# Kernel optimization log

Hardware: AMD Instinct MI355X
Metric: run time of the kernel (lower is better)

The kernel has to match this reference:

```python
import jax, jax.numpy as jnp
import numpy as np

B, T, C, H = 4, 2048, 1024, 16
D = C // H  # head dim = 64


def setup_inputs() -> dict:
    key = jax.random.key(0)
    ks = jax.random.split(key, 5)
    scale = 1.0 / np.sqrt(C)
    return {
        "x": jax.random.normal(ks[0], (B, T, C), dtype=jnp.float32),
        "qkv_w": jax.random.uniform(ks[1], (C, 3 * C), dtype=jnp.float32, minval=-scale, maxval=scale),
        "qkv_b": jax.random.uniform(ks[2], (3 * C,), dtype=jnp.float32, minval=-scale, maxval=scale),
        "out_w": jax.random.uniform(ks[3], (C, C), dtype=jnp.float32, minval=-scale, maxval=scale),
        "out_b": jax.random.uniform(ks[4], (C,), dtype=jnp.float32, minval=-scale, maxval=scale),
    }


def reference(x, qkv_w, qkv_b, out_w, out_b):
    b, t, c = x.shape
    qkv = x @ qkv_w + qkv_b  # [b, t, 3c]
    q, k, v = jnp.split(qkv, 3, axis=-1)
    # [b, h, t, d]
    q = q.reshape(b, t, H, D).transpose(0, 2, 1, 3)
    k = k.reshape(b, t, H, D).transpose(0, 2, 1, 3)
    v = v.reshape(b, t, H, D).transpose(0, 2, 1, 3)
    scores = jnp.einsum("bhqd,bhkd->bhqk", q, k) / jnp.sqrt(jnp.float32(D))
    causal = jnp.tril(jnp.ones((t, t), dtype=bool))
    scores = jnp.where(causal[None, None, :, :], scores, -jnp.inf)
    attn = jax.nn.softmax(scores, axis=-1)
    out = jnp.einsum("bhqk,bhkd->bhqd", attn, v)
    out = out.transpose(0, 2, 1, 3).reshape(b, t, c)
    return out @ out_w + out_b
```

## Files before the change

### kernel.cpp

```cpp
#include <hip/hip_runtime.h>
#include <type_traits>

typedef __bf16 bf16;
typedef __attribute__((ext_vector_type(8))) __bf16 bf16x8;
typedef __attribute__((ext_vector_type(4))) float f32x4;
typedef __attribute__((ext_vector_type(16))) float f32x16;

constexpr int Bc = 4, Tc = 2048, Cc = 1024, Hc = 16;
constexpr int Mrows = Bc * Tc;
constexpr int N3 = 3 * Cc;

#define GLOAD(gp, lp)                                                          \
  __builtin_amdgcn_global_load_lds(                                           \
      (const __attribute__((address_space(1))) void*)(gp),                     \
      (__attribute__((address_space(3))) void*)(lp), 16, 0, 0)

__device__ __forceinline__ uint32_t pk2(float a, float b) {
  uint16_t x = __builtin_bit_cast(uint16_t, (bf16)a);
  uint16_t y = __builtin_bit_cast(uint16_t, (bf16)b);
  return (uint32_t)x | ((uint32_t)y << 16);
}

__global__ __launch_bounds__(256) void cast_bf16_kernel(
    const float* __restrict__ in, bf16* __restrict__ out, int n8) {
  int i = blockIdx.x * blockDim.x + threadIdx.x;
  int stride = gridDim.x * blockDim.x;
  for (; i < n8; i += stride) {
    const float4* p = (const float4*)(in + (long)i * 8);
    float4 a = p[0], b = p[1];
    bf16x8 v;
    v[0] = (bf16)a.x; v[1] = (bf16)a.y; v[2] = (bf16)a.z; v[3] = (bf16)a.w;
    v[4] = (bf16)b.x; v[5] = (bf16)b.y; v[6] = (bf16)b.z; v[7] = (bf16)b.w;
    *(bf16x8*)(out + (long)i * 8) = v;
  }
}

__global__ __launch_bounds__(256) void transpose_cast_kernel(
    const float* __restrict__ in, bf16* __restrict__ out, int rows, int cols,
    float scale, int srows) {
  __shared__ float tile[32][33];
  int tx = threadIdx.x, ty = threadIdx.y;
  int r0 = blockIdx.y * 32, c0 = blockIdx.x * 32;
#pragma unroll
  for (int i = 0; i < 4; i++)
    tile[ty + 8 * i][tx] = in[(long)(r0 + ty + 8 * i) * cols + c0 + tx];
  __syncthreads();
#pragma unroll
  for (int i = 0; i < 4; i++) {
    int orow = c0 + ty + 8 * i;
    float v = tile[tx][ty + 8 * i];
    if (orow < srows) v *= scale;
    out[(long)orow * rows + r0 + tx] = (bf16)v;
  }
}

__global__ __launch_bounds__(256) void transpose_v_kernel(
    const bf16* __restrict__ Y, bf16* __restrict__ Vt) {
  __shared__ bf16 tile[32][33];
  int tx = threadIdx.x, ty = threadIdx.y;
  int t0 = blockIdx.x * 32;
  int d0 = blockIdx.y * 32;
  int bh = blockIdx.z;
  int b = bh >> 4, h = bh & 15;
  const bf16* src = Y + (long)(b * Tc) * N3 + 2 * Cc + h * 64;
#pragma unroll
  for (int i = 0; i < 4; i++)
    tile[ty + 8 * i][tx] = src[(long)(t0 + ty + 8 * i) * N3 + d0 + tx];
  __syncthreads();
  bf16* dst = Vt + (long)bh * 64 * Tc;
  int txp = (tx & 0x13) | ((tx & 4) << 1) | ((tx & 8) >> 1);
#pragma unroll
  for (int i = 0; i < 4; i++)
    dst[(long)(d0 + ty + 8 * i) * Tc + t0 + txp] = tile[tx][ty + 8 * i];
}

template <typename OutT>
__global__ __launch_bounds__(256) void gemm_bt_kernel(
    const bf16* __restrict__ A, const bf16* __restrict__ Bt,
    const float* __restrict__ bias, OutT* __restrict__ Cout, int M, int N,
    int K, int sb) {
  __shared__ __align__(16) bf16 Alds[128 * 32];
  __shared__ __align__(16) bf16 Blds[128 * 32];
  const int tid = threadIdx.x;
  const int w = tid >> 6, l = tid & 63;
  const int m0 = blockIdx.x * 128, n0 = blockIdx.y * 128;
  const int wr = w >> 1, wc = w & 1;
  f32x4 acc[4][4] = {};
  const int arow = tid >> 2, achunk = tid & 3;
  const bf16* Ag = A + (long)(m0 + arow) * K + achunk * 8;
  const bf16* Bg = Bt + (long)(n0 + arow) * K + achunk * 8;
  char* AldsB = (char*)Alds;
  char* BldsB = (char*)Blds;
  const int wbase = w * 1024;

  for (int k0 = 0; k0 < K; k0 += 32) {
    __syncthreads();
    GLOAD(Ag + k0, AldsB + wbase);
    GLOAD(Ag + k0 + (long)64 * K, AldsB + wbase + 4096);
    GLOAD(Bg + k0, BldsB + wbase);
    GLOAD(Bg + k0 + (long)64 * K, BldsB + wbase + 4096);
    __syncthreads();
    const int kk = (l >> 4) * 8;
    bf16x8 af[4], bfr[4];
#pragma unroll
    for (int mi = 0; mi < 4; mi++)
      af[mi] = *(const bf16x8*)(AldsB +
                                ((wr * 64 + mi * 16 + (l & 15)) * 32 + kk) * 2);
#pragma unroll
    for (int ni = 0; ni < 4; ni++)
      bfr[ni] = *(const bf16x8*)(BldsB +
                                 ((wc * 64 + ni * 16 + (l & 15)) * 32 + kk) * 2);
#pragma unroll
    for (int mi = 0; mi < 4; mi++)
#pragma unroll
      for (int ni = 0; ni < 4; ni++)
        acc[mi][ni] = __builtin_amdgcn_mfma_f32_16x16x32_bf16(
            af[mi], bfr[ni], acc[mi][ni], 0, 0, 0);
  }
  const int rrow = (l >> 4) * 4, col = l & 15;
#pragma unroll
  for (int mi = 0; mi < 4; mi++) {
#pragma unroll
    for (int ni = 0; ni < 4; ni++) {
      int gcol = n0 + wc * 64 + ni * 16 + col;
      float bv = bias[gcol];
      if (gcol < sb) bv *= 0.125f;
#pragma unroll
      for (int i = 0; i < 4; i++) {
        int grow = m0 + wr * 64 + mi * 16 + rrow + i;
        float v = acc[mi][ni][i] + bv;
        if constexpr (std::is_same<OutT, float>::value)
          Cout[(long)grow * N + gcol] = v;
        else
          Cout[(long)grow * N + gcol] = (bf16)v;
      }
    }
  }
}

__global__ __launch_bounds__(256) void flash_kernel(
    const bf16* __restrict__ Y, const bf16* __restrict__ Vt,
    bf16* __restrict__ O) {
  __shared__ __align__(16) bf16 Klds[2][64 * 64];
  __shared__ __align__(16) bf16 Vlds[2][64 * 64];
  const int tid = threadIdx.x;
  const int w = tid >> 6, l = tid & 63;
  const int ln = l & 31, hi = l >> 5;
  const int bh = blockIdx.y;
  const int b = bh >> 4, h = bh & 15;
  const bf16* Kbase = Y + (long)(b * Tc) * N3 + Cc + h * 64;
  const bf16* Vbase = Vt + (long)bh * 64 * Tc;

  const int srow = tid >> 3, schunk = tid & 7;
  const int swz = (schunk ^ (srow & 7)) * 8;
  const int wbase = w * 1024;
  char* KldsB = (char*)Klds;
  char* VldsB = (char*)Vlds;

  auto stage = [&](int buf, int kt0) {
    char* kd = KldsB + buf * 8192 + wbase;
    char* vd = VldsB + buf * 8192 + wbase;
    GLOAD(Kbase + (long)(kt0 + srow) * N3 + swz, kd);
    GLOAD(Kbase + (long)(kt0 + srow + 32) * N3 + swz, kd + 4096);
    GLOAD(Vbase + (long)srow * Tc + kt0 + swz, vd);
    GLOAD(Vbase + (long)(srow + 32) * Tc + kt0 + swz, vd + 4096);
  };

#pragma unroll 1
  for (int sp = 0; sp < 2; sp++) {
    const int st = sp ? (15 - (int)blockIdx.x) : (int)blockIdx.x;
    const int q0 = st * 128;
    const int qmin = q0 + w * 32;
    const int qg = qmin + ln;
    const long grow = (long)(b * Tc) + qg;

    bf16x8 aq[4];
#pragma unroll
    for (int dc = 0; dc < 4; dc++)
      aq[dc] = *(const bf16x8*)(Y + grow * N3 + h * 64 + dc * 16 + hi * 8);

    f32x16 ot[2] = {};
    float mrun = -__builtin_inff(), lrun = 0.f;
    const int nkt = 2 * st + 2;

    stage(0, 0);
    __syncthreads();

    for (int kt = 0; kt < nkt; kt++) {
      const int kt0 = kt * 64;
      if (kt + 1 < nkt) stage((kt + 1) & 1, kt0 + 64);
      const char* kb = KldsB + (kt & 1) * 8192;
      const char* vb = VldsB + (kt & 1) * 8192;

      if (kt0 <= qmin + 31) {
        f32x16 s[2];
#pragma unroll
        for (int ks = 0; ks < 2; ks++) {
          f32x16 acc = {};
          const int krow = ks * 32 + ln;
          const int kswz = (krow & 7) << 4;
#pragma unroll
          for (int dc = 0; dc < 4; dc++) {
            bf16x8 ak =
                *(const bf16x8*)(kb + krow * 128 + ((dc * 32 + hi * 16) ^ kswz));
            acc = __builtin_amdgcn_mfma_f32_32x32x16_bf16(ak, aq[dc], acc, 0, 0, 0);
          }
          s[ks] = acc;
        }
        if (kt0 + 63 > qmin) {
#pragma unroll
          for (int ks = 0; ks < 2; ks++)
#pragma unroll
            for (int r = 0; r < 16; r++) {
              int kg = kt0 + ks * 32 + (r & 3) + 8 * (r >> 2) + 4 * hi;
              if (kg > qg) s[ks][r] = -__builtin_inff();
            }
        }
        float tm = s[0][0];
#pragma unroll
        for (int ks = 0; ks < 2; ks++)
#pragma unroll
          for (int r = 0; r < 16; r++) tm = fmaxf(tm, s[ks][r]);
        tm = fmaxf(tm, __shfl_xor(tm, 32));
        float mnew = fmaxf(mrun, tm);
        float factor = __expf(mrun - mnew);
        float lsum = 0.f;
#pragma unroll
        for (int ks = 0; ks < 2; ks++)
#pragma unroll
          for (int r = 0; r < 16; r++) {
            float p = __expf(s[ks][r] - mnew);
            s[ks][r] = p;
            lsum += p;
          }
        lsum += __shfl_xor(lsum, 32);
        lrun = lrun * factor + lsum;
        mrun = mnew;
#pragma unroll
        for (int db = 0; db < 2; db++)
#pragma unroll
          for (int r = 0; r < 16; r++) ot[db][r] *= factor;
        uint32_t pu[2][8];
#pragma unroll
        for (int ks = 0; ks < 2; ks++)
#pragma unroll
          for (int j = 0; j < 8; j++)
            pu[ks][j] = pk2(s[ks][2 * j], s[ks][2 * j + 1]);
#pragma unroll
        for (int ks = 0; ks < 2; ks++)
#pragma unroll
          for (int g = 0; g < 2; g++) {
            union { uint32_t u[4]; bf16x8 v; } pf;
            pf.u[0] = pu[ks][g * 4 + 0];
            pf.u[1] = pu[ks][g * 4 + 1];
            pf.u[2] = pu[ks][g * 4 + 2];
            pf.u[3] = pu[ks][g * 4 + 3];
#pragma unroll
            for (int db = 0; db < 2; db++) {
              const int vrow = db * 32 + ln;
              bf16x8 av = *(const bf16x8*)(
                  vb + vrow * 128 +
                  ((ks * 64 + g * 32 + hi * 16) ^ ((vrow & 7) << 4)));
              ot[db] = __builtin_amdgcn_mfma_f32_32x32x16_bf16(av, pf.v, ot[db],
                                                               0, 0, 0);
            }
          }
      }
      __syncthreads();
    }

    const float sc = 1.f / lrun;
#pragma unroll
    for (int db = 0; db < 2; db++) {
      uint32_t u[8];
#pragma unroll
      for (int j = 0; j < 8; j++)
        u[j] = pk2(ot[db][2 * j] * sc, ot[db][2 * j + 1] * sc);
#pragma unroll
      for (int g = 0; g < 2; g++) {
        uint32_t a0 = u[g * 4 + 0], a1 = u[g * 4 + 1];
        uint32_t a2 = u[g * 4 + 2], a3 = u[g * 4 + 3];
        uint32_t x0 = hi ? a0 : a2, x1 = hi ? a1 : a3;
        uint32_t y0 = (uint32_t)__shfl_xor((int)x0, 32);
        uint32_t y1 = (uint32_t)__shfl_xor((int)x1, 32);
        union { uint32_t u[4]; bf16x8 v; } f;
        f.u[0] = hi ? y0 : a0;
        f.u[1] = hi ? y1 : a1;
        f.u[2] = hi ? a2 : y0;
        f.u[3] = hi ? a3 : y1;
        *(bf16x8*)(O + grow * Cc + h * 64 + db * 32 + g * 16 + hi * 8) = f.v;
      }
    }
  }
}

extern "C" void kernel_launch(void* const* d_in, const int* in_sizes, int n_in,
                              void* d_out, int out_size, void* d_ws,
                              size_t ws_size, hipStream_t stream) {
  const float* x = (const float*)d_in[0];
  const float* qkv_w = (const float*)d_in[1];
  const float* qkv_b = (const float*)d_in[2];
  const float* out_w = (const float*)d_in[3];
  const float* out_b = (const float*)d_in[4];
  float* out = (float*)d_out;
  char* ws = (char*)d_ws;
  bf16* xb = (bf16*)(ws);
  bf16* Obuf = (bf16*)(ws);
  bf16* wqkvT = (bf16*)(ws + (16ull << 20));
  bf16* woT = (bf16*)(ws + (22ull << 20));
  bf16* Ybuf = (bf16*)(ws + (24ull << 20));
  bf16* Vtb = (bf16*)(ws + (72ull << 20));

  cast_bf16_kernel<<<2048, 256, 0, stream>>>(x, xb, Mrows * Cc / 8);
  transpose_cast_kernel<<<dim3(N3 / 32, Cc / 32), dim3(32, 8), 0, stream>>>(
      qkv_w, wqkvT, Cc, N3, 0.125f, Cc);
  transpose_cast_kernel<<<dim3(Cc / 32, Cc / 32), dim3(32, 8), 0, stream>>>(
      out_w, woT, Cc, Cc, 1.0f, 0);
  gemm_bt_kernel<bf16><<<dim3(Mrows / 128, N3 / 128), 256, 0, stream>>>(
      xb, wqkvT, qkv_b, Ybuf, Mrows, N3, Cc, Cc);
  transpose_v_kernel<<<dim3(Tc / 32, 2, Bc * Hc), dim3(32, 8), 0, stream>>>(
      Ybuf, Vtb);
  flash_kernel<<<dim3(8, Bc * Hc), 256, 0, stream>>>(Ybuf, Vtb, Obuf);
  gemm_bt_kernel<float><<<dim3(Mrows / 128, Cc / 128), 256, 0, stream>>>(
      Obuf, woT, out_b, out, Mrows, Cc, Cc, 0);
}
```

Baseline: 278.4 us.

## Replace GEMMs with 8-wave double-buffered pipelined kernel and tile swizzle

Replaces the simple 128x128 single-buffered GEMM with a 512-thread kernel using 256-column (and 256/128-row) tiles. It double-buffers LDS with async global-to-LDS loads, uses explicit vmcnt waits and barriers to overlap loads with MFMA work, and remaps block IDs so neighbouring blocks share tiles. It also raises wave priority around MFMA sections in the GEMM and flash kernels. The hand-scheduled waits and barriers rely on exact counts of outstanding loads, and the larger tiles raise LDS and register pressure.

```diff
diff --git a/kernel.cpp b/kernel.cpp
--- a/kernel.cpp
+++ b/kernel.cpp
@@ -19,6 +19,21 @@
   uint16_t x = __builtin_bit_cast(uint16_t, (bf16)a);
   uint16_t y = __builtin_bit_cast(uint16_t, (bf16)b);
   return (uint32_t)x | ((uint32_t)y << 16);
+}
+
+template <int N>
+__device__ __forceinline__ void vm_wait() {
+  static_assert(N == 3 || N == 4, "");
+  if constexpr (N == 3)
+    asm volatile("s_waitcnt vmcnt(3)" ::: "memory");
+  else
+    asm volatile("s_waitcnt vmcnt(4)" ::: "memory");
+}
+
+__device__ __forceinline__ void barx() {
+  asm volatile("" ::: "memory");
+  __builtin_amdgcn_s_barrier();
+  asm volatile("" ::: "memory");
 }
 
 __global__ __launch_bounds__(256) void cast_bf16_kernel(
@@ -74,68 +89,135 @@
     dst[(long)(d0 + ty + 8 * i) * Tc + t0 + txp] = tile[tx][ty + 8 * i];
 }
 
-template <typename OutT>
-__global__ __launch_bounds__(256) void gemm_bt_kernel(
+template <int BM, typename OutT>
+__global__ __launch_bounds__(512, 2) void gemm8_kernel(
     const bf16* __restrict__ A, const bf16* __restrict__ Bt,
-    const float* __restrict__ bias, OutT* __restrict__ Cout, int M, int N,
-    int K, int sb) {
-  __shared__ __align__(16) bf16 Alds[128 * 32];
-  __shared__ __align__(16) bf16 Blds[128 * 32];
+    const float* __restrict__ bias, OutT* __restrict__ C, int M, int N, int K,
+    int sb, int NMB) {
+  constexpr int MREP = BM / 32;
+  constexpr int ALD = BM / 128;
+  constexpr int VMW = ALD + 2;
+  __shared__ __align__(16) bf16 Abuf[2][2][BM * 32];
+  __shared__ __align__(16) bf16 Bbuf[2][2][256 * 32];
   const int tid = threadIdx.x;
   const int w = tid >> 6, l = tid & 63;
-  const int m0 = blockIdx.x * 128, n0 = blockIdx.y * 128;
-  const int wr = w >> 1, wc = w & 1;
-  f32x4 acc[4][4] = {};
-  const int arow = tid >> 2, achunk = tid & 3;
-  const bf16* Ag = A + (long)(m0 + arow) * K + achunk * 8;
-  const bf16* Bg = Bt + (long)(n0 + arow) * K + achunk * 8;
-  char* AldsB = (char*)Alds;
-  char* BldsB = (char*)Blds;
-  const int wbase = w * 1024;
-
-  for (int k0 = 0; k0 < K; k0 += 32) {
-    __syncthreads();
-    GLOAD(Ag + k0, AldsB + wbase);
-    GLOAD(Ag + k0 + (long)64 * K, AldsB + wbase + 4096);
-    GLOAD(Bg + k0, BldsB + wbase);
-    GLOAD(Bg + k0 + (long)64 * K, BldsB + wbase + 4096);
-    __syncthreads();
-    const int kk = (l >> 4) * 8;
-    bf16x8 af[4], bfr[4];
-#pragma unroll
-    for (int mi = 0; mi < 4; mi++)
-      af[mi] = *(const bf16x8*)(AldsB +
-                                ((wr * 64 + mi * 16 + (l & 15)) * 32 + kk) * 2);
-#pragma unroll
-    for (int ni = 0; ni < 4; ni++)
-      bfr[ni] = *(const bf16x8*)(BldsB +
-                                 ((wc * 64 + ni * 16 + (l & 15)) * 32 + kk) * 2);
-#pragma unroll
-    for (int mi = 0; mi < 4; mi++)
-#pragma unroll
-      for (int ni = 0; ni < 4; ni++)
-        acc[mi][ni] = __builtin_amdgcn_mfma_f32_16x16x32_bf16(
-            af[mi], bfr[ni], acc[mi][ni], 0, 0, 0);
-  }
-  const int rrow = (l >> 4) * 4, col = l & 15;
-#pragma unroll
-  for (int mi = 0; mi < 4; mi++) {
-#pragma unroll
-    for (int ni = 0; ni < 4; ni++) {
-      int gcol = n0 + wc * 64 + ni * 16 + col;
-      float bv = bias[gcol];
-      if (gcol < sb) bv *= 0.125f;
+  const int wm = w >> 2, wn = w & 3;
+  const int lr = l & 15, lc = l >> 4;
+  const int nwg = gridDim.x;
+  const int bid = blockIdx.x;
+  const int swz = (bid & 7) * (nwg >> 3) + (bid >> 3);
+  const int bm = swz % NMB, bn = swz / NMB;
+  const long m0 = (long)bm * BM, n0 = (long)bn * 256;
+  const int NT = K >> 6;
+
+  bf16x8 afA[MREP], afB[MREP], bfX[2], bfY[2];
+  f32x4 acc[MREP][4] = {};
+
+  auto stageA = [&](int nd, int kh, int t) {
+    const bf16* src = A + m0 * K + t * 64 + kh * 32;
+    char* dst = (char*)(&Abuf[nd][kh][0]) + w * 1024;
+#pragma unroll
+    for (int j = 0; j < ALD; j++) {
+      int i = j * 512 + tid;
+      GLOAD(src + (long)(i >> 2) * K + (i & 3) * 8, dst + j * 8192);
+    }
+  };
+  auto stageB = [&](int nd, int kh, int t) {
+    const bf16* src = Bt + n0 * K + t * 64 + kh * 32;
+    char* dst = (char*)(&Bbuf[nd][kh][0]) + w * 1024;
+#pragma unroll
+    for (int j = 0; j < 2; j++) {
+      int i = j * 512 + tid;
+      GLOAD(src + (long)(i >> 2) * K + (i & 3) * 8, dst + j * 8192);
+    }
+  };
+  auto readA = [&](bf16x8 (&af)[MREP], int d, int kh) {
+#pragma unroll
+    for (int mi = 0; mi < MREP; mi++)
+      af[mi] = *(const bf16x8*)(
+          &Abuf[d][kh][(wm * (BM / 2) + mi * 16 + lr) * 32 + lc * 8]);
+  };
+  auto readB = [&](bf16x8 (&bf)[2], int d, int kh, int nh) {
+#pragma unroll
+    for (int nj = 0; nj < 2; nj++)
+      bf[nj] = *(const bf16x8*)(
+          &Bbuf[d][kh][(wn * 64 + (nh * 2 + nj) * 16 + lr) * 32 + lc * 8]);
+  };
+
+#define MMQ(af, bf, NH)                                                        \
+  {                                                                            \
+    __builtin_amdgcn_s_setprio(1);                                             \
+    _Pragma("unroll") for (int mi = 0; mi < MREP; mi++) {                      \
+      acc[mi][NH * 2 + 0] = __builtin_amdgcn_mfma_f32_16x16x32_bf16(           \
+          af[mi], bf[0], acc[mi][NH * 2 + 0], 0, 0, 0);                        \
+      acc[mi][NH * 2 + 1] = __builtin_amdgcn_mfma_f32_16x16x32_bf16(           \
+          af[mi], bf[1], acc[mi][NH * 2 + 1], 0, 0, 0);                        \
+    }                                                                          \
+    __builtin_amdgcn_s_setprio(0);                                             \
+  }
+
+  stageA(0, 0, 0);
+  stageB(0, 0, 0);
+  stageA(0, 1, 0);
+  stageB(0, 1, 0);
+  vm_wait<VMW>();
+  barx();
+  readA(afA, 0, 0);
+  readB(bfX, 0, 0, 0);
+
+  for (int t = 0; t < NT; t++) {
+    const int d = t & 1, nd = d ^ 1;
+    const int tn = (t + 1 < NT) ? t + 1 : t;
+    stageA(nd, 0, tn);
+    barx();
+    readB(bfY, d, 0, 1);
+    __builtin_amdgcn_sched_barrier(0);
+    MMQ(afA, bfX, 0);
+    barx();
+    stageB(nd, 0, tn);
+    vm_wait<VMW>();
+    barx();
+    readA(afB, d, 1);
+    readB(bfX, d, 1, 0);
+    __builtin_amdgcn_sched_barrier(0);
+    MMQ(afA, bfY, 1);
+    barx();
+    stageA(nd, 1, tn);
+    barx();
+    readB(bfY, d, 1, 1);
+    __builtin_amdgcn_sched_barrier(0);
+    MMQ(afB, bfX, 0);
+    barx();
+    stageB(nd, 1, tn);
+    vm_wait<VMW>();
+    barx();
+    readA(afA, nd, 0);
+    readB(bfX, nd, 0, 0);
+    __builtin_amdgcn_sched_barrier(0);
+    MMQ(afB, bfY, 1);
+    barx();
+  }
+  asm volatile("s_waitcnt vmcnt(0)" ::: "memory");
+
+#pragma unroll
+  for (int nc = 0; nc < 4; nc++) {
+    int gcol = (int)n0 + wn * 64 + nc * 16 + lr;
+    float bv = bias[gcol];
+    if (gcol < sb) bv *= 0.125f;
+#pragma unroll
+    for (int mi = 0; mi < MREP; mi++) {
 #pragma unroll
       for (int i = 0; i < 4; i++) {
-        int grow = m0 + wr * 64 + mi * 16 + rrow + i;
-        float v = acc[mi][ni][i] + bv;
+        long grow = m0 + wm * (BM / 2) + mi * 16 + lc * 4 + i;
+        float v = acc[mi][nc][i] + bv;
         if constexpr (std::is_same<OutT, float>::value)
-          Cout[(long)grow * N + gcol] = v;
+          C[grow * N + gcol] = v;
         else
-          Cout[(long)grow * N + gcol] = (bf16)v;
+          C[grow * N + gcol] = (bf16)v;
       }
     }
   }
+#undef MMQ
 }
 
 __global__ __launch_bounds__(256) void flash_kernel(
@@ -194,6 +276,7 @@
 
       if (kt0 <= qmin + 31) {
         f32x16 s[2];
+        __builtin_amdgcn_s_setprio(1);
 #pragma unroll
         for (int ks = 0; ks < 2; ks++) {
           f32x16 acc = {};
@@ -207,6 +290,7 @@
           }
           s[ks] = acc;
         }
+        __builtin_amdgcn_s_setprio(0);
         if (kt0 + 63 > qmin) {
 #pragma unroll
           for (int ks = 0; ks < 2; ks++)
@@ -246,6 +330,7 @@
 #pragma unroll
           for (int j = 0; j < 8; j++)
             pu[ks][j] = pk2(s[ks][2 * j], s[ks][2 * j + 1]);
+        __builtin_amdgcn_s_setprio(1);
 #pragma unroll
         for (int ks = 0; ks < 2; ks++)
 #pragma unroll
@@ -265,6 +350,7 @@
                                                                0, 0, 0);
             }
           }
+        __builtin_amdgcn_s_setprio(0);
       }
       __syncthreads();
     }
@@ -316,11 +402,11 @@
       qkv_w, wqkvT, Cc, N3, 0.125f, Cc);
   transpose_cast_kernel<<<dim3(Cc / 32, Cc / 32), dim3(32, 8), 0, stream>>>(
       out_w, woT, Cc, Cc, 1.0f, 0);
-  gemm_bt_kernel<bf16><<<dim3(Mrows / 128, N3 / 128), 256, 0, stream>>>(
-      xb, wqkvT, qkv_b, Ybuf, Mrows, N3, Cc, Cc);
+  gemm8_kernel<256, bf16><<<384, 512, 0, stream>>>(
+      xb, wqkvT, qkv_b, Ybuf, Mrows, N3, Cc, Cc, Mrows / 256);
   transpose_v_kernel<<<dim3(Tc / 32, 2, Bc * Hc), dim3(32, 8), 0, stream>>>(
       Ybuf, Vtb);
   flash_kernel<<<dim3(8, Bc * Hc), 256, 0, stream>>>(Ybuf, Vtb, Obuf);
-  gemm_bt_kernel<float><<<dim3(Mrows / 128, Cc / 128), 256, 0, stream>>>(
-      Obuf, woT, out_b, out, Mrows, Cc, Cc, 0);
-}
+  gemm8_kernel<128, float><<<256, 512, 0, stream>>>(
+      Obuf, woT, out_b, out, Mrows, Cc, Cc, 0, Mrows / 128);
+}
```

New measurement: 323.2 us. 16.1% more time.

## Deepen GEMM K-tile to 64 with XOR-swizzled LDS and add MFMA priority hints

Applied to the files above, without the earlier changes.

The GEMM kernel now stages a 64-wide K slice per iteration instead of 32, which halves the number of barrier pairs per output tile. LDS rows become 128 bytes, so the column chunk is XOR-swizzled by row to avoid bank conflicts on the fragment reads. The flash attention kernel also wraps its QK and PV MFMA sections in s_setprio to favour matrix issue across waves. The cost is double the LDS per block, which may lower occupancy, and still no overlap between load and compute within the GEMM.

```diff
diff --git a/kernel.cpp b/kernel.cpp
--- a/kernel.cpp
+++ b/kernel.cpp
@@ -79,55 +79,61 @@
     const bf16* __restrict__ A, const bf16* __restrict__ Bt,
     const float* __restrict__ bias, OutT* __restrict__ Cout, int M, int N,
     int K, int sb) {
-  __shared__ __align__(16) bf16 Alds[128 * 32];
-  __shared__ __align__(16) bf16 Blds[128 * 32];
+  __shared__ __align__(16) bf16 Alds[128 * 64];
+  __shared__ __align__(16) bf16 Blds[128 * 64];
   const int tid = threadIdx.x;
   const int w = tid >> 6, l = tid & 63;
   const int m0 = blockIdx.x * 128, n0 = blockIdx.y * 128;
   const int wr = w >> 1, wc = w & 1;
+  const int lr = l & 15, lc = l >> 4;
   f32x4 acc[4][4] = {};
-  const int arow = tid >> 2, achunk = tid & 3;
-  const bf16* Ag = A + (long)(m0 + arow) * K + achunk * 8;
-  const bf16* Bg = Bt + (long)(n0 + arow) * K + achunk * 8;
+  const int srow = tid >> 3;
+  const int csw = (tid & 7) ^ (srow & 7);
+  const bf16* Ag = A + (long)(m0 + srow) * K + csw * 8;
+  const bf16* Bg = Bt + (long)(n0 + srow) * K + csw * 8;
   char* AldsB = (char*)Alds;
   char* BldsB = (char*)Blds;
-  const int wbase = w * 1024;
-
-  for (int k0 = 0; k0 < K; k0 += 32) {
+  const int lbase = tid * 16;
+  const int rswz = (lr & 7) << 4;
+
+  for (int k0 = 0; k0 < K; k0 += 64) {
     __syncthreads();
-    GLOAD(Ag + k0, AldsB + wbase);
-    GLOAD(Ag + k0 + (long)64 * K, AldsB + wbase + 4096);
-    GLOAD(Bg + k0, BldsB + wbase);
-    GLOAD(Bg + k0 + (long)64 * K, BldsB + wbase + 4096);
+#pragma unroll
+    for (int r = 0; r < 4; r++) {
+      GLOAD(Ag + k0 + (long)(r * 32) * K, AldsB + r * 4096 + lbase);
+      GLOAD(Bg + k0 + (long)(r * 32) * K, BldsB + r * 4096 + lbase);
+    }
     __syncthreads();
-    const int kk = (l >> 4) * 8;
-    bf16x8 af[4], bfr[4];
-#pragma unroll
-    for (int mi = 0; mi < 4; mi++)
-      af[mi] = *(const bf16x8*)(AldsB +
-                                ((wr * 64 + mi * 16 + (l & 15)) * 32 + kk) * 2);
-#pragma unroll
-    for (int ni = 0; ni < 4; ni++)
-      bfr[ni] = *(const bf16x8*)(BldsB +
-                                 ((wc * 64 + ni * 16 + (l & 15)) * 32 + kk) * 2);
-#pragma unroll
-    for (int mi = 0; mi < 4; mi++)
+#pragma unroll
+    for (int kk = 0; kk < 2; kk++) {
+      bf16x8 af[4], bfr[4];
+      const int koff = (kk * 64 + lc * 16) ^ rswz;
+#pragma unroll
+      for (int mi = 0; mi < 4; mi++)
+        af[mi] =
+            *(const bf16x8*)(AldsB + (wr * 64 + mi * 16 + lr) * 128 + koff);
 #pragma unroll
       for (int ni = 0; ni < 4; ni++)
-        acc[mi][ni] = __builtin_amdgcn_mfma_f32_16x16x32_bf16(
-            af[mi], bfr[ni], acc[mi][ni], 0, 0, 0);
-  }
-  const int rrow = (l >> 4) * 4, col = l & 15;
+        bfr[ni] =
+            *(const bf16x8*)(BldsB + (wc * 64 + ni * 16 + lr) * 128 + koff);
+#pragma unroll
+      for (int mi = 0; mi < 4; mi++)
+#pragma unroll
+        for (int ni = 0; ni < 4; ni++)
+          acc[mi][ni] = __builtin_amdgcn_mfma_f32_16x16x32_bf16(
+              af[mi], bfr[ni], acc[mi][ni], 0, 0, 0);
+    }
+  }
 #pragma unroll
   for (int mi = 0; mi < 4; mi++) {
 #pragma unroll
     for (int ni = 0; ni < 4; ni++) {
-      int gcol = n0 + wc * 64 + ni * 16 + col;
+      int gcol = n0 + wc * 64 + ni * 16 + lr;
       float bv = bias[gcol];
       if (gcol < sb) bv *= 0.125f;
 #pragma unroll
       for (int i = 0; i < 4; i++) {
-        int grow = m0 + wr * 64 + mi * 16 + rrow + i;
+        int grow = m0 + wr * 64 + mi * 16 + lc * 4 + i;
         float v = acc[mi][ni][i] + bv;
         if constexpr (std::is_same<OutT, float>::value)
           Cout[(long)grow * N + gcol] = v;
@@ -194,6 +200,7 @@
 
       if (kt0 <= qmin + 31) {
         f32x16 s[2];
+        __builtin_amdgcn_s_setprio(1);
 #pragma unroll
         for (int ks = 0; ks < 2; ks++) {
           f32x16 acc = {};
@@ -207,6 +214,7 @@
           }
           s[ks] = acc;
         }
+        __builtin_amdgcn_s_setprio(0);
         if (kt0 + 63 > qmin) {
 #pragma unroll
           for (int ks = 0; ks < 2; ks++)
@@ -246,6 +254,7 @@
 #pragma unroll
           for (int j = 0; j < 8; j++)
             pu[ks][j] = pk2(s[ks][2 * j], s[ks][2 * j + 1]);
+        __builtin_amdgcn_s_setprio(1);
 #pragma unroll
         for (int ks = 0; ks < 2; ks++)
 #pragma unroll
@@ -265,6 +274,7 @@
                                                                0, 0, 0);
             }
           }
+        __builtin_amdgcn_s_setprio(0);
       }
       __syncthreads();
     }
```

After: 274.8 us. Within noise of the previous version (-1.3%).
